# Kernel tuning notes

Hardware: AMD Instinct MI355X
Metric: run time of the kernel (lower is better)

Reference implementation:

```python
import jax, jax.numpy as jnp
import numpy as np

VX, VY = 0.16, 0.16
X_OFFSET = VX / 2 + 0.0      # vx/2 + offset[0]
Y_OFFSET = VY / 2 + (-39.68) # vy/2 + offset[1]
BN_EPS = 1e-5
V, P, C_IN, C_OUT = 40000, 32, 4, 64


def setup_inputs() -> dict:
    key = jax.random.key(0)
    k0, k1, k2, k3 = jax.random.split(key, 4)
    voxels = jax.random.normal(k0, (V, P, C_IN), dtype=jnp.float32)
    num_point_per_voxel = jnp.maximum(
        jax.random.randint(k1, (V,), 0, P + 1), 1).astype(jnp.int32)
    coors = jax.random.randint(k2, (V, 2), 0, 400).astype(jnp.int32)
    W = jax.random.normal(k3, (C_OUT, C_IN + 5), dtype=jnp.float32) * 0.1
    gamma = jnp.ones((C_OUT,), dtype=jnp.float32)
    beta = jnp.zeros((C_OUT,), dtype=jnp.float32)
    return {"voxels": voxels, "num_point_per_voxel": num_point_per_voxel,
            "coors": coors, "W": W, "gamma": gamma, "beta": beta}


def reference(voxels, num_point_per_voxel, coors, W, gamma, beta):
    npts = num_point_per_voxel.astype(voxels.dtype)  # [V]
    xyz = voxels[:, :, :3]
    # cluster offset: subtract per-pillar mean of valid points
    points_mean = jnp.sum(xyz, axis=1, keepdims=True) / npts[:, None, None]
    f_cluster = xyz - points_mean  # [V, P, 3]
    # pillar-center offset
    cx = coors[:, 0].astype(voxels.dtype) * VX + X_OFFSET  # [V]
    cy = coors[:, 1].astype(voxels.dtype) * VY + Y_OFFSET
    f_center = jnp.stack([voxels[:, :, 0] - cx[:, None],
                          voxels[:, :, 1] - cy[:, None]], axis=-1)  # [V, P, 2]
    features = jnp.concatenate([voxels, f_cluster, f_center], axis=-1)  # [V, P, 9]
    # zero out padded points
    point_ids = jnp.arange(P, dtype=jnp.int32)[None, :]
    mask = (num_point_per_voxel[:, None] > point_ids).astype(features.dtype)
    features = features * mask[:, :, None]
    # 1x1 conv == per-point linear: [V, P, 9] x [64, 9] -> [V, P, 64]
    x = jnp.einsum('vpc,oc->vpo', features, W)
    # BatchNorm1d (train mode): stats over (voxel, point) dims per channel
    mean = jnp.mean(x, axis=(0, 1))
    var = jnp.var(x, axis=(0, 1))
    x = (x - mean) * jax.lax.rsqrt(var + BN_EPS) * gamma + beta
    x = jax.nn.relu(x)
    # max over points -> [V, 64]
    return jnp.max(x, axis=1)
```

## Files before the change

kernel.cpp:

```cpp
#include <hip/hip_runtime.h>
#include <hip/hip_bf16.h>

#define V_N   40000
#define P_N   32
#define NTOT  (V_N * P_N)
#define VXc   0.16f
#define VYc   0.16f
#define XOFF  0.08f
#define YOFF  (-39.6f)
#define BN_EPS 1e-5f

#define SBLK  250
#define PBLK  2048
#define PART_OFF  0
#define AFF_OFF   65536
#define MEANS_OFF 73728
#define CY_OFF    (MEANS_OFF + 640000)

#define FOR_S(X) X(0) X(1) X(2) X(3) X(4) X(5) X(6) X(7) X(8)
#define FOR_M(X) \
  X(0,0) X(0,1) X(0,2) X(0,3) X(0,4) X(0,5) X(0,6) X(0,7) X(0,8) \
  X(1,1) X(1,2) X(1,3) X(1,4) X(1,5) X(1,6) X(1,7) X(1,8) \
  X(2,2) X(2,3) X(2,4) X(2,5) X(2,6) X(2,7) X(2,8) \
  X(3,3) X(3,4) X(3,5) X(3,6) X(3,7) X(3,8) \
  X(4,4) X(4,5) X(4,6) X(4,7) X(4,8) \
  X(5,5) X(5,6) X(5,7) X(5,8) \
  X(6,6) X(6,7) X(6,8) \
  X(7,7) X(7,8) \
  X(8,8)

__device__ __forceinline__ float wave_sum(float x) {
#pragma unroll
    for (int m = 1; m < 64; m <<= 1) x += __shfl_xor(x, m, 64);
    return x;
}

__device__ __forceinline__ float rdlane(float x, int l) {
    return __uint_as_float(__builtin_amdgcn_readlane(__float_as_uint(x), l));
}

#define DECL_S(i)   float S##i = 0.f;
#define DECL_M(i,j) float M##i##_##j = 0.f;
#define ACC_S(i)    S##i += f##i;
#define ACC_M(i,j)  M##i##_##j = fmaf(f##i, f##j, M##i##_##j);
#define RED_S(i)    S##i = wave_sum(S##i);
#define RED_M(i,j)  M##i##_##j = wave_sum(M##i##_##j);
#define ST_S(i)     r[k++] = S##i;
#define ST_M(i,j)   r[k++] = M##i##_##j;

#define STAT_BODY(q, v)                                                       \
        {                                                                     \
            float sx = q.x, sy = q.y, sz = q.z;                               \
            _Pragma("unroll")                                                 \
            for (int m = 1; m < 32; m <<= 1) {                                \
                sx += __shfl_xor(sx, m, 64);                                  \
                sy += __shfl_xor(sy, m, 64);                                  \
                sz += __shfl_xor(sz, m, 64);                                  \
            }                                                                 \
            const int   npts = npts_arr[v];                                   \
            const float inv  = 1.f / (float)npts;                             \
            const float mx = sx * inv, my = sy * inv, mz = sz * inv;          \
            const float cx = (float)coors[2 * (v)]     * VXc + XOFF;          \
            const float cy = (float)coors[2 * (v) + 1] * VYc + YOFF;          \
            if (p == 0) { means[v] = make_float4(mx, my, mz, cx);             \
                          cyv[v] = cy; }                                      \
            const float g  = (p < npts) ? 1.f : 0.f;                          \
            const float f0 = q.x * g;                                         \
            const float f1 = q.y * g;                                         \
            const float f2 = q.z * g;                                         \
            const float f3 = q.w * g;                                         \
            const float f4 = (q.x - mx) * g;                                  \
            const float f5 = (q.y - my) * g;                                  \
            const float f6 = (q.z - mz) * g;                                  \
            const float f7 = (q.x - cx) * g;                                  \
            const float f8 = (q.y - cy) * g;                                  \
            FOR_S(ACC_S)                                                      \
            FOR_M(ACC_M)                                                      \
        }

__global__ __launch_bounds__(256) void stats_kernel(
    const float4* __restrict__ voxels,
    const int*    __restrict__ npts_arr,
    const int*    __restrict__ coors,
    float*        __restrict__ ws)
{
    float*  partials = ws;
    float4* means    = (float4*)((char*)ws + MEANS_OFF);
    float*  cyv      = (float*)((char*)ws + CY_OFF);

    const int lane = threadIdx.x & 63;
    const int p    = lane & 31;
    const int half = lane >> 5;
    const int gw   = (blockIdx.x * 256 + threadIdx.x) >> 6;
    const int nw   = (SBLK * 256) >> 6;

    FOR_S(DECL_S)
    FOR_M(DECL_M)

    for (int vb = gw * 4; vb < V_N; vb += nw * 4) {
        const int vA = vb + half;
        const int vB = vb + 2 + half;
        float4 q1 = voxels[(size_t)vA * P_N + p];
        float4 q2 = voxels[(size_t)vB * P_N + p];
        STAT_BODY(q1, vA)
        STAT_BODY(q2, vB)
    }

    FOR_S(RED_S)
    FOR_M(RED_M)

    __shared__ float red[4][54];
    const int wib = threadIdx.x >> 6;
    if (lane == 0) {
        float* r = red[wib];
        int k = 0;
        FOR_S(ST_S)
        FOR_M(ST_M)
    }
    __syncthreads();
    if (threadIdx.x < 64) {
        float s = 0.f;
        if (threadIdx.x < 54)
            s = red[0][threadIdx.x] + red[1][threadIdx.x]
              + red[2][threadIdx.x] + red[3][threadIdx.x];
        partials[blockIdx.x * 64 + threadIdx.x] = s;
    }
}

__global__ __launch_bounds__(256) void affine_kernel(
    const float* __restrict__ W,
    const float* __restrict__ gamma,
    const float* __restrict__ beta,
    float*       __restrict__ ws)
{
    const float* partials = ws;
    float*       aff      = (float*)((char*)ws + AFF_OFF);

    __shared__ float red2[4][64];
    __shared__ float stc[64];

    const int c   = threadIdx.x & 63;
    const int seg = threadIdx.x >> 6;

    float s = 0.f;
    for (int r = seg; r < SBLK; r += 4)
        s += partials[r * 64 + c];
    red2[seg][c] = s;
    __syncthreads();
    if (threadIdx.x < 64)
        stc[threadIdx.x] = red2[0][threadIdx.x] + red2[1][threadIdx.x]
                         + red2[2][threadIdx.x] + red2[3][threadIdx.x];
    __syncthreads();

    if (threadIdx.x < 64) {
        const int o = threadIdx.x;
        float w[9];
#pragma unroll
        for (int cc = 0; cc < 9; ++cc) w[cc] = W[o * 9 + cc];

        const float invN = 1.f / (float)NTOT;
        float mean = 0.f;
#pragma unroll
        for (int cc = 0; cc < 9; ++cc) mean = fmaf(w[cc], stc[cc], mean);
        mean *= invN;

        float ex2 = 0.f;
        int k = 9;
#pragma unroll
        for (int i = 0; i < 9; ++i)
#pragma unroll
            for (int j = i; j < 9; ++j) {
                const float coef = (i == j) ? 1.f : 2.f;
                ex2 = fmaf(coef * w[i] * w[j], stc[k], ex2);
                ++k;
            }
        ex2 *= invN;
        const float var   = ex2 - mean * mean;
        const float scale = gamma[o] * rsqrtf(var + BN_EPS);
        const float bias  = fmaf(-mean, scale, beta[o]);

        aff[0 * 64 + o] = (w[0] + w[4] + w[7]) * scale;
        aff[1 * 64 + o] = (w[1] + w[5] + w[8]) * scale;
        aff[2 * 64 + o] = (w[2] + w[6]) * scale;
        aff[3 * 64 + o] =  w[3] * scale;
        aff[4 * 64 + o] =  w[4] * scale;
        aff[5 * 64 + o] =  w[5] * scale;
        aff[6 * 64 + o] =  w[6] * scale;
        aff[7 * 64 + o] =  w[7] * scale;
        aff[8 * 64 + o] =  w[8] * scale;
        aff[9 * 64 + o] =  bias;
    }
}

__global__ __launch_bounds__(256) void pfn_kernel(
    const float4* __restrict__ voxels,
    const int*    __restrict__ npts_arr,
    const float*  __restrict__ ws,
    float*        __restrict__ out)
{
    const float*  aff   = (const float*)((const char*)ws + AFF_OFF);
    const float4* means = (const float4*)((const char*)ws + MEANS_OFF);
    const float*  cyv   = (const float*)((const char*)ws + CY_OFF);

    const int lane = threadIdx.x & 63;
    const int wib  = threadIdx.x >> 6;

    const float a0   = aff[0 * 64 + lane];
    const float a1   = aff[1 * 64 + lane];
    const float a2   = aff[2 * 64 + lane];
    const float a3   = aff[3 * 64 + lane];
    const float u4   = aff[4 * 64 + lane];
    const float u5   = aff[5 * 64 + lane];
    const float u6   = aff[6 * 64 + lane];
    const float u7   = aff[7 * 64 + lane];
    const float u8   = aff[8 * 64 + lane];
    const float bias = aff[9 * 64 + lane];

    const int gwave = blockIdx.x * 4 + wib;

#define DOT(P_, OFS_) \
    fmaf(rdlane(q.x, (P_) + (OFS_)), a0, \
    fmaf(rdlane(q.y, (P_) + (OFS_)), a1, \
    fmaf(rdlane(q.z, (P_) + (OFS_)), a2, \
         rdlane(q.w, (P_) + (OFS_)) * a3)))

    for (int pr = gwave; pr < V_N / 2; pr += PBLK * 4) {
        const int vA = pr * 2;
        const int vB = vA + 1;

        const int vv = vA + (lane >> 5);
        const float4 q = voxels[(size_t)vv * P_N + (lane & 31)];

        const int nA = __builtin_amdgcn_readfirstlane(npts_arr[vA]);
        const int nB = __builtin_amdgcn_readfirstlane(npts_arr[vB]);

        const float4 mA = means[vA];
        const float4 mB = means[vB];
        const float cyA = cyv[vA];
        const float cyB = cyv[vB];

        const float bA = -fmaf(mA.x, u4, fmaf(mA.y, u5, fmaf(mA.z, u6,
                           fmaf(mA.w, u7, cyA * u8))));
        const float bB = -fmaf(mB.x, u4, fmaf(mB.y, u5, fmaf(mB.z, u6,
                           fmaf(mB.w, u7, cyB * u8))));

        float e0 = -3.4e38f, e1 = -3.4e38f;
        {
            int p = 0;
            for (; p + 1 < nA; p += 2) {
                const float d0 = DOT(p, 0);
                const float d1 = DOT(p + 1, 0);
                e0 = fmaxf(e0, d0);
                e1 = fmaxf(e1, d1);
            }
            if (p < nA) e0 = fmaxf(e0, DOT(p, 0));
        }
        float mfA = fmaxf(e0, e1) + bA;
        if (nA < P_N) mfA = fmaxf(mfA, 0.f);
        out[(size_t)vA * 64 + lane] = fmaxf(mfA + bias, 0.f);

        float g0 = -3.4e38f, g1 = -3.4e38f;
        {
            int p = 0;
            for (; p + 1 < nB; p += 2) {
                const float d0 = DOT(p, 32);
                const float d1 = DOT(p + 1, 32);
                g0 = fmaxf(g0, d0);
                g1 = fmaxf(g1, d1);
            }
            if (p < nB) g0 = fmaxf(g0, DOT(p, 32));
        }
        float mfB = fmaxf(g0, g1) + bB;
        if (nB < P_N) mfB = fmaxf(mfB, 0.f);
        out[(size_t)vB * 64 + lane] = fmaxf(mfB + bias, 0.f);
    }
#undef DOT
}

extern "C" void kernel_launch(void* const* d_in, const int* in_sizes, int n_in,
                              void* d_out, int out_size, void* d_ws, size_t ws_size,
                              hipStream_t stream)
{
    const float4* voxels = (const float4*)d_in[0];
    const int*    npts   = (const int*)d_in[1];
    const int*    coors  = (const int*)d_in[2];
    const float*  W      = (const float*)d_in[3];
    const float*  gamma  = (const float*)d_in[4];
    const float*  beta   = (const float*)d_in[5];
    float*        out    = (float*)d_out;
    float*        ws     = (float*)d_ws;

    stats_kernel <<<SBLK, 256, 0, stream>>>(voxels, npts, coors, ws);
    affine_kernel<<<1,    256, 0, stream>>>(W, gamma, beta, ws);
    pfn_kernel   <<<PBLK, 256, 0, stream>>>(voxels, npts, ws, out);
}
```

Measured before the change: 127.7 us.

## Fold affine kernel into pfn via sharded atomic stats and per-block recompute

```diff
diff --git a/kernel.cpp b/kernel.cpp
--- a/kernel.cpp
+++ b/kernel.cpp
@@ -11,11 +11,11 @@
 #define BN_EPS 1e-5f
 
 #define SBLK  250
-#define PBLK  2048
-#define PART_OFF  0
-#define AFF_OFF   65536
-#define MEANS_OFF 73728
-#define CY_OFF    (MEANS_OFF + 640000)
+#define PBLK  2500
+#define NSHARD 8
+#define CNT_BYTES  (54 * NSHARD * 32 * 4)
+#define MEANS_OFF  57344
+#define CY_OFF     (MEANS_OFF + V_N * 16)
 
 #define FOR_S(X) X(0) X(1) X(2) X(3) X(4) X(5) X(6) X(7) X(8)
 #define FOR_M(X) \
@@ -84,9 +84,9 @@
     const int*    __restrict__ coors,
     float*        __restrict__ ws)
 {
-    float*  partials = ws;
-    float4* means    = (float4*)((char*)ws + MEANS_OFF);
-    float*  cyv      = (float*)((char*)ws + CY_OFF);
+    float*  cnt   = ws;
+    float4* means = (float4*)((char*)ws + MEANS_OFF);
+    float*  cyv   = (float*)((char*)ws + CY_OFF);
 
     const int lane = threadIdx.x & 63;
     const int p    = lane & 31;
@@ -118,50 +118,50 @@
         FOR_M(ST_M)
     }
     __syncthreads();
-    if (threadIdx.x < 64) {
+    if (threadIdx.x < 54) {
+        float s = red[0][threadIdx.x] + red[1][threadIdx.x]
+                + red[2][threadIdx.x] + red[3][threadIdx.x];
+        atomicAdd(&cnt[(threadIdx.x * NSHARD + (blockIdx.x & (NSHARD - 1))) * 32], s);
+    }
+}
+
+__global__ __launch_bounds__(256) void pfn_kernel(
+    const float4* __restrict__ voxels,
+    const int*    __restrict__ npts_arr,
+    const float*  __restrict__ W,
+    const float*  __restrict__ gamma,
+    const float*  __restrict__ beta,
+    const float*  __restrict__ ws,
+    float*        __restrict__ out)
+{
+    const float*  cnt   = ws;
+    const float4* means = (const float4*)((const char*)ws + MEANS_OFF);
+    const float*  cyv   = (const float*)((const char*)ws + CY_OFF);
+
+    __shared__ float stc[54];
+    __shared__ float affs[10][64];
+
+    const int lane = threadIdx.x & 63;
+    const int wib  = threadIdx.x >> 6;
+
+    if (threadIdx.x < 54) {
         float s = 0.f;
-        if (threadIdx.x < 54)
-            s = red[0][threadIdx.x] + red[1][threadIdx.x]
-              + red[2][threadIdx.x] + red[3][threadIdx.x];
-        partials[blockIdx.x * 64 + threadIdx.x] = s;
-    }
-}
-
-__global__ __launch_bounds__(256) void affine_kernel(
-    const float* __restrict__ W,
-    const float* __restrict__ gamma,
-    const float* __restrict__ beta,
-    float*       __restrict__ ws)
-{
-    const float* partials = ws;
-    float*       aff      = (float*)((char*)ws + AFF_OFF);
-
-    __shared__ float red2[4][64];
-    __shared__ float stc[64];
-
-    const int c   = threadIdx.x & 63;
-    const int seg = threadIdx.x >> 6;
-
-    float s = 0.f;
-    for (int r = seg; r < SBLK; r += 4)
-        s += partials[r * 64 + c];
-    red2[seg][c] = s;
+#pragma unroll
+        for (int sh = 0; sh < NSHARD; ++sh)
+            s += cnt[(threadIdx.x * NSHARD + sh) * 32];
+        stc[threadIdx.x] = s;
+    }
     __syncthreads();
-    if (threadIdx.x < 64)
-        stc[threadIdx.x] = red2[0][threadIdx.x] + red2[1][threadIdx.x]
-                         + red2[2][threadIdx.x] + red2[3][threadIdx.x];
-    __syncthreads();
-
     if (threadIdx.x < 64) {
         const int o = threadIdx.x;
         float w[9];
 #pragma unroll
-        for (int cc = 0; cc < 9; ++cc) w[cc] = W[o * 9 + cc];
+        for (int c = 0; c < 9; ++c) w[c] = W[o * 9 + c];
 
         const float invN = 1.f / (float)NTOT;
         float mean = 0.f;
 #pragma unroll
-        for (int cc = 0; cc < 9; ++cc) mean = fmaf(w[cc], stc[cc], mean);
+        for (int c = 0; c < 9; ++c) mean = fmaf(w[c], stc[c], mean);
         mean *= invN;
 
         float ex2 = 0.f;
@@ -179,42 +179,29 @@
         const float scale = gamma[o] * rsqrtf(var + BN_EPS);
         const float bias  = fmaf(-mean, scale, beta[o]);
 
-        aff[0 * 64 + o] = (w[0] + w[4] + w[7]) * scale;
-        aff[1 * 64 + o] = (w[1] + w[5] + w[8]) * scale;
-        aff[2 * 64 + o] = (w[2] + w[6]) * scale;
-        aff[3 * 64 + o] =  w[3] * scale;
-        aff[4 * 64 + o] =  w[4] * scale;
-        aff[5 * 64 + o] =  w[5] * scale;
-        aff[6 * 64 + o] =  w[6] * scale;
-        aff[7 * 64 + o] =  w[7] * scale;
-        aff[8 * 64 + o] =  w[8] * scale;
-        aff[9 * 64 + o] =  bias;
-    }
-}
-
-__global__ __launch_bounds__(256) void pfn_kernel(
-    const float4* __restrict__ voxels,
-    const int*    __restrict__ npts_arr,
-    const float*  __restrict__ ws,
-    float*        __restrict__ out)
-{
-    const float*  aff   = (const float*)((const char*)ws + AFF_OFF);
-    const float4* means = (const float4*)((const char*)ws + MEANS_OFF);
-    const float*  cyv   = (const float*)((const char*)ws + CY_OFF);
-
-    const int lane = threadIdx.x & 63;
-    const int wib  = threadIdx.x >> 6;
-
-    const float a0   = aff[0 * 64 + lane];
-    const float a1   = aff[1 * 64 + lane];
-    const float a2   = aff[2 * 64 + lane];
-    const float a3   = aff[3 * 64 + lane];
-    const float u4   = aff[4 * 64 + lane];
-    const float u5   = aff[5 * 64 + lane];
-    const float u6   = aff[6 * 64 + lane];
-    const float u7   = aff[7 * 64 + lane];
-    const float u8   = aff[8 * 64 + lane];
-    const float bias = aff[9 * 64 + lane];
+        affs[0][o] = (w[0] + w[4] + w[7]) * scale;
+        affs[1][o] = (w[1] + w[5] + w[8]) * scale;
+        affs[2][o] = (w[2] + w[6]) * scale;
+        affs[3][o] =  w[3] * scale;
+        affs[4][o] =  w[4] * scale;
+        affs[5][o] =  w[5] * scale;
+        affs[6][o] =  w[6] * scale;
+        affs[7][o] =  w[7] * scale;
+        affs[8][o] =  w[8] * scale;
+        affs[9][o] =  bias;
+    }
+    __syncthreads();
+
+    const float a0   = affs[0][lane];
+    const float a1   = affs[1][lane];
+    const float a2   = affs[2][lane];
+    const float a3   = affs[3][lane];
+    const float u4   = affs[4][lane];
+    const float u5   = affs[5][lane];
+    const float u6   = affs[6][lane];
+    const float u7   = affs[7][lane];
+    const float u8   = affs[8][lane];
+    const float bias = affs[9][lane];
 
     const int gwave = blockIdx.x * 4 + wib;
 
@@ -224,8 +211,9 @@
     fmaf(rdlane(q.z, (P_) + (OFS_)), a2, \
          rdlane(q.w, (P_) + (OFS_)) * a3)))
 
-    for (int pr = gwave; pr < V_N / 2; pr += PBLK * 4) {
-        const int vA = pr * 2;
+#pragma unroll
+    for (int it = 0; it < 2; ++it) {
+        const int vA = gwave * 4 + it * 2;
         const int vB = vA + 1;
 
         const int vv = vA + (lane >> 5);
@@ -246,14 +234,14 @@
 
         float e0 = -3.4e38f, e1 = -3.4e38f;
         {
-            int p = 0;
-            for (; p + 1 < nA; p += 2) {
-                const float d0 = DOT(p, 0);
-                const float d1 = DOT(p + 1, 0);
+            int pp = 0;
+            for (; pp + 1 < nA; pp += 2) {
+                const float d0 = DOT(pp, 0);
+                const float d1 = DOT(pp + 1, 0);
                 e0 = fmaxf(e0, d0);
                 e1 = fmaxf(e1, d1);
             }
-            if (p < nA) e0 = fmaxf(e0, DOT(p, 0));
+            if (pp < nA) e0 = fmaxf(e0, DOT(pp, 0));
         }
         float mfA = fmaxf(e0, e1) + bA;
         if (nA < P_N) mfA = fmaxf(mfA, 0.f);
@@ -261,14 +249,14 @@
 
         float g0 = -3.4e38f, g1 = -3.4e38f;
         {
-            int p = 0;
-            for (; p + 1 < nB; p += 2) {
-                const float d0 = DOT(p, 32);
-                const float d1 = DOT(p + 1, 32);
+            int pp = 0;
+            for (; pp + 1 < nB; pp += 2) {
+                const float d0 = DOT(pp, 32);
+                const float d1 = DOT(pp + 1, 32);
                 g0 = fmaxf(g0, d0);
                 g1 = fmaxf(g1, d1);
             }
-            if (p < nB) g0 = fmaxf(g0, DOT(p, 32));
+            if (pp < nB) g0 = fmaxf(g0, DOT(pp, 32));
         }
         float mfB = fmaxf(g0, g1) + bB;
         if (nB < P_N) mfB = fmaxf(mfB, 0.f);
@@ -290,7 +278,7 @@
     float*        out    = (float*)d_out;
     float*        ws     = (float*)d_ws;
 
-    stats_kernel <<<SBLK, 256, 0, stream>>>(voxels, npts, coors, ws);
-    affine_kernel<<<1,    256, 0, stream>>>(W, gamma, beta, ws);
-    pfn_kernel   <<<PBLK, 256, 0, stream>>>(voxels, npts, ws, out);
-}
+    hipMemsetAsync(d_ws, 0, CNT_BYTES, stream);
+    stats_kernel<<<SBLK, 256, 0, stream>>>(voxels, npts, coors, ws);
+    pfn_kernel  <<<PBLK, 256, 0, stream>>>(voxels, npts, W, gamma, beta, ws, out);
+}
```

Result: faster. 115.7 us (-9.4%).
